# Optimization experiments

Measured on AMD Instinct MI355X. Metric: run time of the kernel, lower is better.

The kernel has to match this reference:

```python
import jax, jax.numpy as jnp
import numpy as np

B, N, F, H = 4, 40, 128, 128  # batch, num_nodes, in_features, hidden_features


def setup_inputs() -> dict:
    key = jax.random.key(0)
    ks = jax.random.split(key, 8)
    s = 0.02
    lengths = jax.random.randint(ks[0], (B,), N // 2, N + 1)
    mask = jnp.arange(N)[None, :] < lengths[:, None]  # (B, N) bool padding mask
    return dict(
        x=jax.random.normal(ks[1], (B, N, N, N, F), jnp.float32),
        mask=mask,
        Wi1=jax.random.normal(ks[2], (F, F), jnp.float32) * s, bi1=jnp.zeros((F,), jnp.float32),
        Wi2=jax.random.normal(ks[3], (F, H), jnp.float32) * s, bi2=jnp.zeros((H,), jnp.float32),
        We=jax.random.normal(ks[4], (H, H), jnp.float32) * s,
        Wo1=jax.random.normal(ks[5], (2 * H, 2 * H), jnp.float32) * s, bo1=jnp.zeros((2 * H,), jnp.float32),
        Wo2=jax.random.normal(ks[6], (2 * H, 1), jnp.float32) * s, bo2=jnp.zeros((1,), jnp.float32),
    )


def reference(x, mask, Wi1, bi1, Wi2, bi2, We, Wo1, bo1, Wo2, bo2):
    b, n = x.shape[0], x.shape[1]
    # inner MLP: F -> H, applied per hyperedge (B, n, n, n, H)
    x_embed = jnp.maximum(x @ Wi1 + bi1, 0.0) @ Wi2 + bi2
    # hyperedge validity: all three nodes unpadded AND strict ordering i < j < k
    idx = jnp.arange(n)
    ijk = (idx[:, None, None] < idx[None, :, None]) & (idx[None, :, None] < idx[None, None, :])  # (n,n,n)
    hm = (mask[:, :, None, None] & mask[:, None, :, None] & mask[:, None, None, :]) & ijk[None]  # (B,n,n,n)
    xf = x_embed.reshape(b, n * n * n, H)  # (B, n^3, H)
    logits = jnp.where(hm.reshape(b, n * n * n, 1), xf, -jnp.inf)
    a_flat = jax.nn.softmax(logits, axis=1)  # softmax over all n^3 hyperedges, per channel
    x_inner = jnp.maximum(xf @ We, 0.0)  # (B, n^3, H)
    h = jnp.concatenate([a_flat * x_inner, xf], axis=-1)  # (B, n^3, 2H)
    out = jnp.maximum(h @ Wo1 + bo1, 0.0) @ Wo2 + bo2  # (B, n^3, 1)
    return out.reshape(b, n, n, n)
```

## Files before the change

kernel.cpp:

```cpp
#include <hip/hip_runtime.h>

#define Bn 4
#define Nn 40
#define NCUBE 64000
#define ROWS 128
#define BPB  500
#define SROWS 64
#define SBPB 1000
#define MAXV 16384
#define CBLK 160

typedef _Float16 f16;
typedef __attribute__((ext_vector_type(8)))  _Float16 f16x8;
typedef __attribute__((ext_vector_type(4)))  _Float16 f16x4;
typedef __attribute__((ext_vector_type(4)))  float    f32x4;
typedef __attribute__((ext_vector_type(16))) float    f32x16;

#define OFF_WI1 0
#define OFF_WI2 16384
#define OFF_WE  32768
#define OFF_WO1 49152
#define WB_HALFS 114688
#define WB_BYTES (WB_HALFS*2)
#define WBOFF_COMPACT (4096 + Bn*MAXV*4)
#define WBOFF_SMALL   2560

__device__ __forceinline__ int swz8(int row, int colg) {
    return row*256 + (((colg & ~7) | ((colg ^ row) & 7)) << 3);
}
__device__ __forceinline__ int swzofs(int row, int col) {
    return swz8(row, col >> 3) + (col & 7);
}

template<bool PRE>
__device__ __forceinline__ f16x8 load_wfrag(const f16* __restrict__ WF,
                                            const float* __restrict__ W,
                                            int N, int NT, int kt, int nt, int l) {
    if constexpr (PRE) {
        return *(const f16x8*)(WF + ((kt*NT + nt)*64 + l)*8);
    } else {
        const int col = nt*32 + (l & 31);
        const int k0  = kt*16 + 8*(l >> 5);
        f16x8 r;
        #pragma unroll
        for (int j = 0; j < 8; ++j) r[j] = (f16)W[(k0 + j)*N + col];
        return r;
    }
}

__device__ __forceinline__ f16x8 lds_af(const f16* hb, int rowbase, int areag, int kt, int l) {
    return *(const f16x8*)&hb[swz8(rowbase + (l & 31), areag + 2*kt + (l >> 5))];
}

__global__ __launch_bounds__(256)
void prepcount_kernel(const float* __restrict__ Wi1, const float* __restrict__ Wi2,
                      const float* __restrict__ We,  const float* __restrict__ Wo1,
                      f16* __restrict__ WB, const unsigned char* __restrict__ mask,
                      int* __restrict__ cnt, int* __restrict__ vlist) {
    const int blk = blockIdx.x;
    if (blk < 56) {
        int id = blk*256 + threadIdx.x;
        const float* W; int NT, N; f16* WF; int fid;
        if (id < 2048)      { W = Wi1; NT = 4; N = 128; WF = WB+OFF_WI1; fid = id; }
        else if (id < 4096) { W = Wi2; NT = 4; N = 128; WF = WB+OFF_WI2; fid = id-2048; }
        else if (id < 6144) { W = We;  NT = 4; N = 128; WF = WB+OFF_WE;  fid = id-4096; }
        else                { W = Wo1; NT = 8; N = 256; WF = WB+OFF_WO1; fid = id-6144; }
        int frag = fid >> 6, l = fid & 63;
        int nt = frag % NT, kt = frag / NT;
        int col = nt*32 + (l & 31), k0 = kt*16 + 8*(l >> 5);
        #pragma unroll
        for (int j = 0; j < 8; ++j) WF[frag*512 + l*8 + j] = (f16)W[(k0 + j)*N + col];
    } else {
        const int idx = (blk - 56)*256 + threadIdx.x;
        const int b = idx / NCUBE, e = idx % NCUBE;
        const int k = e % Nn, ij = e / Nn, j = ij % Nn, i = ij / Nn;
        const bool v = (i < j) && (j < k) &&
                       mask[b*Nn+i] && mask[b*Nn+j] && mask[b*Nn+k];
        const unsigned long long m = __ballot(v);
        const int lane = threadIdx.x & 63;
        const int c = __popcll(m);
        int base = 0;
        if (lane == 0 && c) base = atomicAdd(&cnt[b], c);
        base = __shfl(base, 0);
        if (v) vlist[b*MAXV + base + __popcll(m & ((1ull<<lane)-1ull))] = e;
    }
}

template<bool PRE, bool COMPACT>
__global__ __launch_bounds__(512, 4)
void sums_kernel(const float* __restrict__ x, const unsigned char* __restrict__ mask,
                 const float* __restrict__ Wi1, const float* __restrict__ bi1,
                 const float* __restrict__ Wi2, const float* __restrict__ bi2,
                 float* __restrict__ sums, const int* __restrict__ cnt,
                 const int* __restrict__ vlist, const f16* __restrict__ WB)
{
    const int tid = threadIdx.x;
    const int l = tid & 63, w = tid >> 6, lr = l & 31, lh = l >> 5;
    const int wr = w >> 2, wc = w & 3;
    int b, r0;
    if (COMPACT) { b = blockIdx.x / CBLK; r0 = (blockIdx.x % CBLK)*SROWS; if (r0 >= cnt[b]) return; }
    else         { b = blockIdx.x / SBPB; r0 = (blockIdx.x % SBPB)*SROWS; }

    __shared__ __align__(16) f16 hb[SROWS*256];
    __shared__ int earr[SROWS];
    __shared__ unsigned char mlds[Nn];
    __shared__ int anyv;

    if (!COMPACT) { if (tid < Nn) mlds[tid] = mask[b*Nn + tid]; if (tid == 0) anyv = 0; }
    if (tid < SROWS) {
        if (COMPACT) { int r = r0 + tid; earr[tid] = (r < cnt[b]) ? vlist[b*MAXV + r] : -1; }
        else earr[tid] = r0 + tid;
    }
    __syncthreads();

    bool rv;
    {
        int e = earr[32*wr + lr];
        if (!COMPACT) {
            int k = e % Nn, ij = e / Nn, j = ij % Nn, i = ij / Nn;
            rv = (i < j) && (j < k) && mlds[i] && mlds[j] && mlds[k];
            if (__any(rv)) anyv = 1;
            __syncthreads();
            if (!anyv) return;
        } else rv = (e >= 0);
    }

    #pragma unroll
    for (int p = 0; p < 2; ++p) {
        const int row = p*32 + (tid >> 4);
        const int c0  = (tid & 15)*8;
        int e = earr[row]; if (e < 0) e = 0;
        const float4 x0 = *(const float4*)&x[((long)(b*NCUBE + e))*128 + c0];
        const float4 x1 = *(const float4*)&x[((long)(b*NCUBE + e))*128 + c0 + 4];
        f16x8 v; v[0]=(f16)x0.x; v[1]=(f16)x0.y; v[2]=(f16)x0.z; v[3]=(f16)x0.w;
                 v[4]=(f16)x1.x; v[5]=(f16)x1.y; v[6]=(f16)x1.z; v[7]=(f16)x1.w;
        *(f16x8*)&hb[swzofs(row, 128 + c0)] = v;
    }
    __syncthreads();

    f32x16 acc;
    #pragma unroll
    for (int rg = 0; rg < 4; ++rg) {
        const float4 bv = *(const float4*)(bi1 + 32*wc + 8*rg + 4*lh);
        acc[rg*4+0]=bv.x; acc[rg*4+1]=bv.y; acc[rg*4+2]=bv.z; acc[rg*4+3]=bv.w;
    }
    #pragma unroll
    for (int kt = 0; kt < 8; ++kt) {
        const f16x8 wf = load_wfrag<PRE>(WB+OFF_WI1, Wi1, 128, 4, kt, wc, l);
        const f16x8 af = lds_af(hb, 32*wr, 16, kt, l);
        acc = __builtin_amdgcn_mfma_f32_32x32x16_f16(wf, af, acc, 0, 0, 0);
    }
    #pragma unroll
    for (int rg = 0; rg < 4; ++rg) {
        f16x4 v;
        #pragma unroll
        for (int q = 0; q < 4; ++q) v[q] = (f16)fmaxf(acc[rg*4+q], 0.f);
        *(f16x4*)&hb[swzofs(32*wr + lr, 32*wc + 8*rg + 4*lh)] = v;
    }
    __syncthreads();

    #pragma unroll
    for (int rg = 0; rg < 4; ++rg) {
        const float4 bv = *(const float4*)(bi2 + 32*wc + 8*rg + 4*lh);
        acc[rg*4+0]=bv.x; acc[rg*4+1]=bv.y; acc[rg*4+2]=bv.z; acc[rg*4+3]=bv.w;
    }
    #pragma unroll
    for (int kt = 0; kt < 8; ++kt) {
        const f16x8 wf = load_wfrag<PRE>(WB+OFF_WI2, Wi2, 128, 4, kt, wc, l);
        const f16x8 af = lds_af(hb, 32*wr, 0, kt, l);
        acc = __builtin_amdgcn_mfma_f32_32x32x16_f16(wf, af, acc, 0, 0, 0);
    }

    float s[16];
    #pragma unroll
    for (int r = 0; r < 16; ++r) s[r] = rv ? __expf(acc[r]) : 0.0f;
    #pragma unroll
    for (int r = 0; r < 16; ++r) {
        float v = s[r];
        v += __shfl_xor(v, 1); v += __shfl_xor(v, 2);
        v += __shfl_xor(v, 4); v += __shfl_xor(v, 8); v += __shfl_xor(v, 16);
        if (lr == 0) atomicAdd(&sums[b*128 + 32*wc + 8*(r>>2) + 4*lh + (r&3)], v);
    }
}

template<bool PRE>
__global__ __launch_bounds__(512, 4)
void full_kernel(const float* __restrict__ x, const unsigned char* __restrict__ mask,
                 const float* __restrict__ Wi1, const float* __restrict__ bi1,
                 const float* __restrict__ Wi2, const float* __restrict__ bi2,
                 const float* __restrict__ We,
                 const float* __restrict__ Wo1, const float* __restrict__ bo1,
                 const float* __restrict__ Wo2, const float* __restrict__ bo2,
                 const float* __restrict__ sums, const f16* __restrict__ WB,
                 float* __restrict__ out)
{
    const int tid = threadIdx.x;
    const int l = tid & 63, w = tid >> 6, lr = l & 31, lh = l >> 5;
    const int wr = w >> 2, wc = w & 3;
    const int b = blockIdx.x / BPB;
    const int e0 = (blockIdx.x % BPB) * ROWS;

    __shared__ __align__(16) f16 hb[ROWS*256];
    __shared__ float red[8][64];
    __shared__ unsigned char mlds[Nn];

    if (tid < Nn) mlds[tid] = mask[b*Nn + tid];

    #pragma unroll
    for (int p = 0; p < 4; ++p) {
        const int row = p*32 + (tid >> 4);
        const int c0  = (tid & 15)*8;
        const long base = ((long)(b*NCUBE + e0 + row))*128 + c0;
        const float4 x0 = *(const float4*)&x[base];
        const float4 x1 = *(const float4*)&x[base + 4];
        f16x8 v; v[0]=(f16)x0.x; v[1]=(f16)x0.y; v[2]=(f16)x0.z; v[3]=(f16)x0.w;
                 v[4]=(f16)x1.x; v[5]=(f16)x1.y; v[6]=(f16)x1.z; v[7]=(f16)x1.w;
        *(f16x8*)&hb[swzofs(row, 128 + c0)] = v;
    }
    __syncthreads();

    bool valid[2];
    #pragma unroll
    for (int mt = 0; mt < 2; ++mt) {
        int e = e0 + 64*wr + 32*mt + lr;
        int k = e % Nn, ij = e / Nn, j = ij % Nn, i = ij / Nn;
        valid[mt] = (i < j) && (j < k) && mlds[i] && mlds[j] && mlds[k];
    }

    {
        f32x16 acc1[2];
        #pragma unroll
        for (int rg = 0; rg < 4; ++rg) {
            const float4 bv = *(const float4*)(bi1 + 32*wc + 8*rg + 4*lh);
            #pragma unroll
            for (int mt = 0; mt < 2; ++mt) {
                acc1[mt][rg*4+0]=bv.x; acc1[mt][rg*4+1]=bv.y;
                acc1[mt][rg*4+2]=bv.z; acc1[mt][rg*4+3]=bv.w;
            }
        }
        #pragma unroll
        for (int kt = 0; kt < 8; ++kt) {
            const f16x8 wf = load_wfrag<PRE>(WB+OFF_WI1, Wi1, 128, 4, kt, wc, l);
            #pragma unroll
            for (int mt = 0; mt < 2; ++mt) {
                const f16x8 af = lds_af(hb, 64*wr + 32*mt, 16, kt, l);
                acc1[mt] = __builtin_amdgcn_mfma_f32_32x32x16_f16(wf, af, acc1[mt], 0, 0, 0);
            }
        }
        #pragma unroll
        for (int mt = 0; mt < 2; ++mt)
            #pragma unroll
            for (int rg = 0; rg < 4; ++rg) {
                f16x4 v;
                #pragma unroll
                for (int q = 0; q < 4; ++q) v[q] = (f16)fmaxf(acc1[mt][rg*4+q], 0.f);
                *(f16x4*)&hb[swzofs(64*wr + 32*mt + lr, 32*wc + 8*rg + 4*lh)] = v;
            }
    }
    __syncthreads();

    f32x16 acc2[2];
    {
        #pragma unroll
        for (int rg = 0; rg < 4; ++rg) {
            const float4 bv = *(const float4*)(bi2 + 32*wc + 8*rg + 4*lh);
            #pragma unroll
            for (int mt = 0; mt < 2; ++mt) {
                acc2[mt][rg*4+0]=bv.x; acc2[mt][rg*4+1]=bv.y;
                acc2[mt][rg*4+2]=bv.z; acc2[mt][rg*4+3]=bv.w;
            }
        }
        #pragma unroll
        for (int kt = 0; kt < 8; ++kt) {
            const f16x8 wf = load_wfrag<PRE>(WB+OFF_WI2, Wi2, 128, 4, kt, wc, l);
            #pragma unroll
            for (int mt = 0; mt < 2; ++mt) {
                const f16x8 af = lds_af(hb, 64*wr + 32*mt, 0, kt, l);
                acc2[mt] = __builtin_amdgcn_mfma_f32_32x32x16_f16(wf, af, acc2[mt], 0, 0, 0);
            }
        }
        #pragma unroll
        for (int mt = 0; mt < 2; ++mt)
            #pragma unroll
            for (int rg = 0; rg < 4; ++rg) {
                f16x4 v;
                #pragma unroll
                for (int q = 0; q < 4; ++q) v[q] = (f16)acc2[mt][rg*4+q];
                *(f16x4*)&hb[swzofs(64*wr + 32*mt + lr, 128 + 32*wc + 8*rg + 4*lh)] = v;
            }
        #pragma unroll
        for (int rg = 0; rg < 4; ++rg) {
            const float4 sv = *(const float4*)(sums + b*128 + 32*wc + 8*rg + 4*lh);
            const float rinv[4] = {1.f/sv.x, 1.f/sv.y, 1.f/sv.z, 1.f/sv.w};
            #pragma unroll
            for (int mt = 0; mt < 2; ++mt)
                #pragma unroll
                for (int q = 0; q < 4; ++q)
                    acc2[mt][rg*4+q] = valid[mt] ? __expf(acc2[mt][rg*4+q]) * rinv[q] : 0.0f;
        }
    }
    __syncthreads();

    {
        f32x16 acc3[2];
        #pragma unroll
        for (int mt = 0; mt < 2; ++mt)
            #pragma unroll
            for (int r = 0; r < 16; ++r) acc3[mt][r] = 0.f;
        #pragma unroll
        for (int kt = 0; kt < 8; ++kt) {
            const f16x8 wf = load_wfrag<PRE>(WB+OFF_WE, We, 128, 4, kt, wc, l);
            #pragma unroll
            for (int mt = 0; mt < 2; ++mt) {
                const f16x8 af = lds_af(hb, 64*wr + 32*mt, 16, kt, l);
                acc3[mt] = __builtin_amdgcn_mfma_f32_32x32x16_f16(wf, af, acc3[mt], 0, 0, 0);
            }
        }
        #pragma unroll
        for (int mt = 0; mt < 2; ++mt)
            #pragma unroll
            for (int rg = 0; rg < 4; ++rg) {
                f16x4 v;
                #pragma unroll
                for (int q = 0; q < 4; ++q)
                    v[q] = (f16)(acc2[mt][rg*4+q] * fmaxf(acc3[mt][rg*4+q], 0.f));
                *(f16x4*)&hb[swzofs(64*wr + 32*mt + lr, 32*wc + 8*rg + 4*lh)] = v;
            }
    }
    __syncthreads();

    f32x16 acc4[2][2];
    #pragma unroll
    for (int ntl = 0; ntl < 2; ++ntl)
        #pragma unroll
        for (int rg = 0; rg < 4; ++rg) {
            const float4 bv = *(const float4*)(bo1 + 64*wc + 32*ntl + 8*rg + 4*lh);
            #pragma unroll
            for (int mt = 0; mt < 2; ++mt) {
                acc4[mt][ntl][rg*4+0]=bv.x; acc4[mt][ntl][rg*4+1]=bv.y;
                acc4[mt][ntl][rg*4+2]=bv.z; acc4[mt][ntl][rg*4+3]=bv.w;
            }
        }
    #pragma unroll
    for (int kt = 0; kt < 16; ++kt) {
        f16x8 of0 = load_wfrag<PRE>(WB+OFF_WO1, Wo1, 256, 8, kt, 2*wc+0, l);
        f16x8 of1 = load_wfrag<PRE>(WB+OFF_WO1, Wo1, 256, 8, kt, 2*wc+1, l);
        #pragma unroll
        for (int mt = 0; mt < 2; ++mt) {
            const f16x8 af = lds_af(hb, 64*wr + 32*mt, 0, kt, l);
            acc4[mt][0] = __builtin_amdgcn_mfma_f32_32x32x16_f16(of0, af, acc4[mt][0], 0, 0, 0);
            acc4[mt][1] = __builtin_amdgcn_mfma_f32_32x32x16_f16(of1, af, acc4[mt][1], 0, 0, 0);
        }
    }

    {
        float outp[2] = {0.f, 0.f};
        #pragma unroll
        for (int ntl = 0; ntl < 2; ++ntl)
            #pragma unroll
            for (int rg = 0; rg < 4; ++rg) {
                const float4 wv = *(const float4*)(Wo2 + 64*wc + 32*ntl + 8*rg + 4*lh);
                #pragma unroll
                for (int mt = 0; mt < 2; ++mt) {
                    outp[mt] += fmaxf(acc4[mt][ntl][rg*4+0], 0.f)*wv.x
                              + fmaxf(acc4[mt][ntl][rg*4+1], 0.f)*wv.y
                              + fmaxf(acc4[mt][ntl][rg*4+2], 0.f)*wv.z
                              + fmaxf(acc4[mt][ntl][rg*4+3], 0.f)*wv.w;
                }
            }
        #pragma unroll
        for (int mt = 0; mt < 2; ++mt) outp[mt] += __shfl_xor(outp[mt], 32);
        if (l < 32) {
            red[w][lr]      = outp[0];
            red[w][32 + lr] = outp[1];
        }
        __syncthreads();
        if (tid < ROWS) {
            const int wr2 = tid >> 6, idx = tid & 63;
            out[(long)b*NCUBE + e0 + tid] =
                red[wr2*4+0][idx] + red[wr2*4+1][idx] +
                red[wr2*4+2][idx] + red[wr2*4+3][idx] + bo2[0];
        }
    }
}

extern "C" void kernel_launch(void* const* d_in, const int* in_sizes, int n_in,
                              void* d_out, int out_size, void* d_ws, size_t ws_size,
                              hipStream_t stream) {
    const float*         x    = (const float*)d_in[0];
    const unsigned char* mask = (const unsigned char*)d_in[1];
    const float* Wi1 = (const float*)d_in[2];
    const float* bi1 = (const float*)d_in[3];
    const float* Wi2 = (const float*)d_in[4];
    const float* bi2 = (const float*)d_in[5];
    const float* We  = (const float*)d_in[6];
    const float* Wo1 = (const float*)d_in[7];
    const float* bo1 = (const float*)d_in[8];
    const float* Wo2 = (const float*)d_in[9];
    const float* bo2 = (const float*)d_in[10];
    float* out  = (float*)d_out;
    float* sums = (float*)d_ws;
    int*   cnt   = (int*)((char*)d_ws + 2048);
    int*   vlist = (int*)((char*)d_ws + 4096);

    const bool compact = ws_size >= (size_t)(WBOFF_COMPACT + WB_BYTES);
    const size_t wboff = compact ? WBOFF_COMPACT : WBOFF_SMALL;
    const bool pre     = ws_size >= wboff + WB_BYTES;
    f16* WB = (f16*)((char*)d_ws + wboff);

    hipMemsetAsync(d_ws, 0, 2048 + Bn*sizeof(int), stream);

    if (compact) {
        prepcount_kernel<<<1056, 256, 0, stream>>>(Wi1, Wi2, We, Wo1, WB, mask, cnt, vlist);
        sums_kernel<true, true><<<Bn*CBLK, 512, 0, stream>>>(x, mask, Wi1, bi1, Wi2, bi2,
                                                             sums, cnt, vlist, WB);
        full_kernel<true><<<Bn*BPB, 512, 0, stream>>>(x, mask, Wi1, bi1, Wi2, bi2, We,
                                                      Wo1, bo1, Wo2, bo2, sums, WB, out);
    } else if (pre) {
        prepcount_kernel<<<56, 256, 0, stream>>>(Wi1, Wi2, We, Wo1, WB, mask, cnt, vlist);
        sums_kernel<true, false><<<Bn*SBPB, 512, 0, stream>>>(x, mask, Wi1, bi1, Wi2, bi2,
                                                              sums, cnt, vlist, WB);
        full_kernel<true><<<Bn*BPB, 512, 0, stream>>>(x, mask, Wi1, bi1, Wi2, bi2, We,
                                                      Wo1, bo1, Wo2, bo2, sums, WB, out);
    } else {
        sums_kernel<false, false><<<Bn*SBPB, 512, 0, stream>>>(x, mask, Wi1, bi1, Wi2, bi2,
                                                               sums, cnt, vlist, WB);
        full_kernel<false><<<Bn*BPB, 512, 0, stream>>>(x, mask, Wi1, bi1, Wi2, bi2, We,
                                                       Wo1, bo1, Wo2, bo2, sums, WB, out);
    }
}
```

Measured before the change: 271.1 us.

## Compute embeddings once and store fp16 xf to workspace for output pass

Replaces the compacted valid-row sums pass with an embed kernel that reads x once for every row, computes the inner MLP, accumulates the softmax denominators and writes the fp16 embeddings to a large workspace buffer. A new output kernel reads those fp16 embeddings instead of re-reading the fp32 x and recomputing the inner MLP. This removes the second fp32 read of x and the duplicated Wi1/Wi2 GEMMs. In exchange it needs a workspace of about 65 MB plus an extra fp16 write and read, and the embed pass now covers all rows rather than only the valid ones.

```diff
diff --git a/kernel.cpp b/kernel.cpp
--- a/kernel.cpp
+++ b/kernel.cpp
@@ -7,13 +7,10 @@
 #define BPB  500
 #define SROWS 64
 #define SBPB 1000
-#define MAXV 16384
-#define CBLK 160
 
 typedef _Float16 f16;
 typedef __attribute__((ext_vector_type(8)))  _Float16 f16x8;
 typedef __attribute__((ext_vector_type(4)))  _Float16 f16x4;
-typedef __attribute__((ext_vector_type(4)))  float    f32x4;
 typedef __attribute__((ext_vector_type(16))) float    f32x16;
 
 #define OFF_WI1 0
@@ -22,8 +19,10 @@
 #define OFF_WO1 49152
 #define WB_HALFS 114688
 #define WB_BYTES (WB_HALFS*2)
-#define WBOFF_COMPACT (4096 + Bn*MAXV*4)
-#define WBOFF_SMALL   2560
+#define XF_BYTES (Bn*NCUBE*128*2)
+#define WBOFF_BIG (2048 + XF_BYTES)
+#define WS_BIG    (WBOFF_BIG + WB_BYTES)
+#define WBOFF_SMALL 2560
 
 __device__ __forceinline__ int swz8(int row, int colg) {
     return row*256 + (((colg & ~7) | ((colg ^ row) & 7)) << 3);
@@ -52,86 +51,282 @@
     return *(const f16x8*)&hb[swz8(rowbase + (l & 31), areag + 2*kt + (l >> 5))];
 }
 
+__device__ __forceinline__ bool row_valid(int e, const unsigned char* mlds) {
+    int k = e % Nn, ij = e / Nn, j = ij % Nn, i = ij / Nn;
+    return (i < j) && (j < k) && mlds[i] && mlds[j] && mlds[k];
+}
+
 __global__ __launch_bounds__(256)
-void prepcount_kernel(const float* __restrict__ Wi1, const float* __restrict__ Wi2,
-                      const float* __restrict__ We,  const float* __restrict__ Wo1,
-                      f16* __restrict__ WB, const unsigned char* __restrict__ mask,
-                      int* __restrict__ cnt, int* __restrict__ vlist) {
-    const int blk = blockIdx.x;
-    if (blk < 56) {
-        int id = blk*256 + threadIdx.x;
-        const float* W; int NT, N; f16* WF; int fid;
-        if (id < 2048)      { W = Wi1; NT = 4; N = 128; WF = WB+OFF_WI1; fid = id; }
-        else if (id < 4096) { W = Wi2; NT = 4; N = 128; WF = WB+OFF_WI2; fid = id-2048; }
-        else if (id < 6144) { W = We;  NT = 4; N = 128; WF = WB+OFF_WE;  fid = id-4096; }
-        else                { W = Wo1; NT = 8; N = 256; WF = WB+OFF_WO1; fid = id-6144; }
-        int frag = fid >> 6, l = fid & 63;
-        int nt = frag % NT, kt = frag / NT;
-        int col = nt*32 + (l & 31), k0 = kt*16 + 8*(l >> 5);
-        #pragma unroll
-        for (int j = 0; j < 8; ++j) WF[frag*512 + l*8 + j] = (f16)W[(k0 + j)*N + col];
-    } else {
-        const int idx = (blk - 56)*256 + threadIdx.x;
-        const int b = idx / NCUBE, e = idx % NCUBE;
-        const int k = e % Nn, ij = e / Nn, j = ij % Nn, i = ij / Nn;
-        const bool v = (i < j) && (j < k) &&
-                       mask[b*Nn+i] && mask[b*Nn+j] && mask[b*Nn+k];
-        const unsigned long long m = __ballot(v);
-        const int lane = threadIdx.x & 63;
-        const int c = __popcll(m);
-        int base = 0;
-        if (lane == 0 && c) base = atomicAdd(&cnt[b], c);
-        base = __shfl(base, 0);
-        if (v) vlist[b*MAXV + base + __popcll(m & ((1ull<<lane)-1ull))] = e;
-    }
-}
-
-template<bool PRE, bool COMPACT>
+void prep_kernel(const float* __restrict__ Wi1, const float* __restrict__ Wi2,
+                 const float* __restrict__ We,  const float* __restrict__ Wo1,
+                 f16* __restrict__ WB) {
+    int id = blockIdx.x*256 + threadIdx.x;
+    const float* W; int NT, N; f16* WF; int fid;
+    if (id < 2048)      { W = Wi1; NT = 4; N = 128; WF = WB+OFF_WI1; fid = id; }
+    else if (id < 4096) { W = Wi2; NT = 4; N = 128; WF = WB+OFF_WI2; fid = id-2048; }
+    else if (id < 6144) { W = We;  NT = 4; N = 128; WF = WB+OFF_WE;  fid = id-4096; }
+    else                { W = Wo1; NT = 8; N = 256; WF = WB+OFF_WO1; fid = id-6144; }
+    int frag = fid >> 6, l = fid & 63;
+    int nt = frag % NT, kt = frag / NT;
+    int col = nt*32 + (l & 31), k0 = kt*16 + 8*(l >> 5);
+    #pragma unroll
+    for (int j = 0; j < 8; ++j) WF[frag*512 + l*8 + j] = (f16)W[(k0 + j)*N + col];
+}
+
+template<bool PRE>
+__global__ __launch_bounds__(512, 4)
+void embed_kernel(const float* __restrict__ x, const unsigned char* __restrict__ mask,
+                  const float* __restrict__ Wi1, const float* __restrict__ bi1,
+                  const float* __restrict__ Wi2, const float* __restrict__ bi2,
+                  float* __restrict__ sums, f16* __restrict__ xfg,
+                  const f16* __restrict__ WB)
+{
+    const int tid = threadIdx.x;
+    const int l = tid & 63, w = tid >> 6, lr = l & 31, lh = l >> 5;
+    const int wr = w >> 2, wc = w & 3;
+    const int b = blockIdx.x / SBPB;
+    const int e0 = (blockIdx.x % SBPB) * SROWS;
+
+    __shared__ __align__(16) f16 hb[SROWS*256];
+    __shared__ unsigned char mlds[Nn];
+
+    if (tid < Nn) mlds[tid] = mask[b*Nn + tid];
+
+    #pragma unroll
+    for (int p = 0; p < 2; ++p) {
+        const int row = p*32 + (tid >> 4);
+        const int c0  = (tid & 15)*8;
+        const long base = ((long)(b*NCUBE + e0 + row))*128 + c0;
+        const float4 x0 = *(const float4*)&x[base];
+        const float4 x1 = *(const float4*)&x[base + 4];
+        f16x8 v; v[0]=(f16)x0.x; v[1]=(f16)x0.y; v[2]=(f16)x0.z; v[3]=(f16)x0.w;
+                 v[4]=(f16)x1.x; v[5]=(f16)x1.y; v[6]=(f16)x1.z; v[7]=(f16)x1.w;
+        *(f16x8*)&hb[swzofs(row, 128 + c0)] = v;
+    }
+    __syncthreads();
+
+    const bool rv = row_valid(e0 + 32*wr + lr, mlds);
+
+    f32x16 acc;
+    #pragma unroll
+    for (int rg = 0; rg < 4; ++rg) {
+        const float4 bv = *(const float4*)(bi1 + 32*wc + 8*rg + 4*lh);
+        acc[rg*4+0]=bv.x; acc[rg*4+1]=bv.y; acc[rg*4+2]=bv.z; acc[rg*4+3]=bv.w;
+    }
+    #pragma unroll
+    for (int kt = 0; kt < 8; ++kt) {
+        const f16x8 wf = load_wfrag<PRE>(WB+OFF_WI1, Wi1, 128, 4, kt, wc, l);
+        const f16x8 af = lds_af(hb, 32*wr, 16, kt, l);
+        acc = __builtin_amdgcn_mfma_f32_32x32x16_f16(wf, af, acc, 0, 0, 0);
+    }
+    #pragma unroll
+    for (int rg = 0; rg < 4; ++rg) {
+        f16x4 v;
+        #pragma unroll
+        for (int q = 0; q < 4; ++q) v[q] = (f16)fmaxf(acc[rg*4+q], 0.f);
+        *(f16x4*)&hb[swzofs(32*wr + lr, 32*wc + 8*rg + 4*lh)] = v;
+    }
+    __syncthreads();
+
+    #pragma unroll
+    for (int rg = 0; rg < 4; ++rg) {
+        const float4 bv = *(const float4*)(bi2 + 32*wc + 8*rg + 4*lh);
+        acc[rg*4+0]=bv.x; acc[rg*4+1]=bv.y; acc[rg*4+2]=bv.z; acc[rg*4+3]=bv.w;
+    }
+    #pragma unroll
+    for (int kt = 0; kt < 8; ++kt) {
+        const f16x8 wf = load_wfrag<PRE>(WB+OFF_WI2, Wi2, 128, 4, kt, wc, l);
+        const f16x8 af = lds_af(hb, 32*wr, 0, kt, l);
+        acc = __builtin_amdgcn_mfma_f32_32x32x16_f16(wf, af, acc, 0, 0, 0);
+    }
+
+    float s[16];
+    #pragma unroll
+    for (int rg = 0; rg < 4; ++rg) {
+        f16x4 v;
+        #pragma unroll
+        for (int q = 0; q < 4; ++q) {
+            v[q] = (f16)acc[rg*4+q];
+            s[rg*4+q] = rv ? __expf((float)v[q]) : 0.0f;
+        }
+        *(f16x4*)&hb[swzofs(32*wr + lr, 128 + 32*wc + 8*rg + 4*lh)] = v;
+    }
+    #pragma unroll
+    for (int r = 0; r < 16; ++r) {
+        float v = s[r];
+        v += __shfl_xor(v, 1); v += __shfl_xor(v, 2);
+        v += __shfl_xor(v, 4); v += __shfl_xor(v, 8); v += __shfl_xor(v, 16);
+        if (lr == 0) atomicAdd(&sums[b*128 + 32*wc + 8*(r>>2) + 4*lh + (r&3)], v);
+    }
+    __syncthreads();
+
+    #pragma unroll
+    for (int p = 0; p < 2; ++p) {
+        const int row = p*32 + (tid >> 4);
+        const int c0  = (tid & 15)*8;
+        const f16x8 v = *(const f16x8*)&hb[swzofs(row, 128 + c0)];
+        *(f16x8*)&xfg[((long)(b*NCUBE + e0 + row))*128 + c0] = v;
+    }
+}
+
+template<bool PRE>
+__global__ __launch_bounds__(512, 4)
+void out_kernel(const f16* __restrict__ xfg, const unsigned char* __restrict__ mask,
+                const float* __restrict__ We,
+                const float* __restrict__ Wo1, const float* __restrict__ bo1,
+                const float* __restrict__ Wo2, const float* __restrict__ bo2,
+                const float* __restrict__ sums, const f16* __restrict__ WB,
+                float* __restrict__ out)
+{
+    const int tid = threadIdx.x;
+    const int l = tid & 63, w = tid >> 6, lr = l & 31, lh = l >> 5;
+    const int wr = w >> 2, wc = w & 3;
+    const int b = blockIdx.x / BPB;
+    const int e0 = (blockIdx.x % BPB) * ROWS;
+
+    __shared__ __align__(16) f16 hb[ROWS*256];
+    __shared__ float red[8][64];
+    __shared__ unsigned char mlds[Nn];
+
+    if (tid < Nn) mlds[tid] = mask[b*Nn + tid];
+
+    #pragma unroll
+    for (int p = 0; p < 4; ++p) {
+        const int row = p*32 + (tid >> 4);
+        const int c0  = (tid & 15)*8;
+        const f16x8 v = *(const f16x8*)&xfg[((long)(b*NCUBE + e0 + row))*128 + c0];
+        *(f16x8*)&hb[swzofs(row, 128 + c0)] = v;
+    }
+    __syncthreads();
+
+    bool valid[2];
+    #pragma unroll
+    for (int mt = 0; mt < 2; ++mt)
+        valid[mt] = row_valid(e0 + 64*wr + 32*mt + lr, mlds);
+
+    {
+        f32x16 acc3[2];
+        #pragma unroll
+        for (int mt = 0; mt < 2; ++mt)
+            #pragma unroll
+            for (int r = 0; r < 16; ++r) acc3[mt][r] = 0.f;
+        #pragma unroll
+        for (int kt = 0; kt < 8; ++kt) {
+            const f16x8 wf = load_wfrag<PRE>(WB+OFF_WE, We, 128, 4, kt, wc, l);
+            #pragma unroll
+            for (int mt = 0; mt < 2; ++mt) {
+                const f16x8 af = lds_af(hb, 64*wr + 32*mt, 16, kt, l);
+                acc3[mt] = __builtin_amdgcn_mfma_f32_32x32x16_f16(wf, af, acc3[mt], 0, 0, 0);
+            }
+        }
+        #pragma unroll
+        for (int rg = 0; rg < 4; ++rg) {
+            const float4 sv = *(const float4*)(sums + b*128 + 32*wc + 8*rg + 4*lh);
+            const float rinv[4] = {1.f/sv.x, 1.f/sv.y, 1.f/sv.z, 1.f/sv.w};
+            #pragma unroll
+            for (int mt = 0; mt < 2; ++mt) {
+                const f16x4 xq = *(const f16x4*)&hb[swzofs(64*wr + 32*mt + lr,
+                                                           128 + 32*wc + 8*rg + 4*lh)];
+                f16x4 v;
+                #pragma unroll
+                for (int q = 0; q < 4; ++q) {
+                    const float aa = valid[mt] ? __expf((float)xq[q]) * rinv[q] : 0.0f;
+                    v[q] = (f16)(aa * fmaxf(acc3[mt][rg*4+q], 0.f));
+                }
+                *(f16x4*)&hb[swzofs(64*wr + 32*mt + lr, 32*wc + 8*rg + 4*lh)] = v;
+            }
+        }
+    }
+    __syncthreads();
+
+    f32x16 acc4[2][2];
+    #pragma unroll
+    for (int ntl = 0; ntl < 2; ++ntl)
+        #pragma unroll
+        for (int rg = 0; rg < 4; ++rg) {
+            const float4 bv = *(const float4*)(bo1 + 64*wc + 32*ntl + 8*rg + 4*lh);
+            #pragma unroll
+            for (int mt = 0; mt < 2; ++mt) {
+                acc4[mt][ntl][rg*4+0]=bv.x; acc4[mt][ntl][rg*4+1]=bv.y;
+                acc4[mt][ntl][rg*4+2]=bv.z; acc4[mt][ntl][rg*4+3]=bv.w;
+            }
+        }
+    #pragma unroll
+    for (int kt = 0; kt < 16; ++kt) {
+        f16x8 of0 = load_wfrag<PRE>(WB+OFF_WO1, Wo1, 256, 8, kt, 2*wc+0, l);
+        f16x8 of1 = load_wfrag<PRE>(WB+OFF_WO1, Wo1, 256, 8, kt, 2*wc+1, l);
+        #pragma unroll
+        for (int mt = 0; mt < 2; ++mt) {
+            const f16x8 af = lds_af(hb, 64*wr + 32*mt, 0, kt, l);
+            acc4[mt][0] = __builtin_amdgcn_mfma_f32_32x32x16_f16(of0, af, acc4[mt][0], 0, 0, 0);
+            acc4[mt][1] = __builtin_amdgcn_mfma_f32_32x32x16_f16(of1, af, acc4[mt][1], 0, 0, 0);
+        }
+    }
+
+    {
+        float outp[2] = {0.f, 0.f};
+        #pragma unroll
+        for (int ntl = 0; ntl < 2; ++ntl)
+            #pragma unroll
+            for (int rg = 0; rg < 4; ++rg) {
+                const float4 wv = *(const float4*)(Wo2 + 64*wc + 32*ntl + 8*rg + 4*lh);
+                #pragma unroll
+                for (int mt = 0; mt < 2; ++mt) {
+                    outp[mt] += fmaxf(acc4[mt][ntl][rg*4+0], 0.f)*wv.x
+                              + fmaxf(acc4[mt][ntl][rg*4+1], 0.f)*wv.y
+                              + fmaxf(acc4[mt][ntl][rg*4+2], 0.f)*wv.z
+                              + fmaxf(acc4[mt][ntl][rg*4+3], 0.f)*wv.w;
+                }
+            }
+        #pragma unroll
+        for (int mt = 0; mt < 2; ++mt) outp[mt] += __shfl_xor(outp[mt], 32);
+        if (l < 32) {
+            red[w][lr]      = outp[0];
+            red[w][32 + lr] = outp[1];
+        }
+        __syncthreads();
+        if (tid < ROWS) {
+            const int wr2 = tid >> 6, idx = tid & 63;
+            out[(long)b*NCUBE + e0 + tid] =
+                red[wr2*4+0][idx] + red[wr2*4+1][idx] +
+                red[wr2*4+2][idx] + red[wr2*4+3][idx] + bo2[0];
+        }
+    }
+}
+
+template<bool PRE>
 __global__ __launch_bounds__(512, 4)
 void sums_kernel(const float* __restrict__ x, const unsigned char* __restrict__ mask,
                  const float* __restrict__ Wi1, const float* __restrict__ bi1,
                  const float* __restrict__ Wi2, const float* __restrict__ bi2,
-                 float* __restrict__ sums, const int* __restrict__ cnt,
-                 const int* __restrict__ vlist, const f16* __restrict__ WB)
+                 float* __restrict__ sums, const f16* __restrict__ WB)
 {
     const int tid = threadIdx.x;
     const int l = tid & 63, w = tid >> 6, lr = l & 31, lh = l >> 5;
     const int wr = w >> 2, wc = w & 3;
-    int b, r0;
-    if (COMPACT) { b = blockIdx.x / CBLK; r0 = (blockIdx.x % CBLK)*SROWS; if (r0 >= cnt[b]) return; }
-    else         { b = blockIdx.x / SBPB; r0 = (blockIdx.x % SBPB)*SROWS; }
+    const int b = blockIdx.x / SBPB;
+    const int e0 = (blockIdx.x % SBPB) * SROWS;
 
     __shared__ __align__(16) f16 hb[SROWS*256];
-    __shared__ int earr[SROWS];
     __shared__ unsigned char mlds[Nn];
     __shared__ int anyv;
 
-    if (!COMPACT) { if (tid < Nn) mlds[tid] = mask[b*Nn + tid]; if (tid == 0) anyv = 0; }
-    if (tid < SROWS) {
-        if (COMPACT) { int r = r0 + tid; earr[tid] = (r < cnt[b]) ? vlist[b*MAXV + r] : -1; }
-        else earr[tid] = r0 + tid;
-    }
-    __syncthreads();
-
-    bool rv;
-    {
-        int e = earr[32*wr + lr];
-        if (!COMPACT) {
-            int k = e % Nn, ij = e / Nn, j = ij % Nn, i = ij / Nn;
-            rv = (i < j) && (j < k) && mlds[i] && mlds[j] && mlds[k];
-            if (__any(rv)) anyv = 1;
-            __syncthreads();
-            if (!anyv) return;
-        } else rv = (e >= 0);
-    }
+    if (tid < Nn) mlds[tid] = mask[b*Nn + tid];
+    if (tid == 0) anyv = 0;
+    __syncthreads();
+
+    const bool rv = row_valid(e0 + 32*wr + lr, mlds);
+    if (__any(rv)) anyv = 1;
+    __syncthreads();
+    if (!anyv) return;
 
     #pragma unroll
     for (int p = 0; p < 2; ++p) {
         const int row = p*32 + (tid >> 4);
         const int c0  = (tid & 15)*8;
-        int e = earr[row]; if (e < 0) e = 0;
-        const float4 x0 = *(const float4*)&x[((long)(b*NCUBE + e))*128 + c0];
-        const float4 x1 = *(const float4*)&x[((long)(b*NCUBE + e))*128 + c0 + 4];
+        const long base = ((long)(b*NCUBE + e0 + row))*128 + c0;
+        const float4 x0 = *(const float4*)&x[base];
+        const float4 x1 = *(const float4*)&x[base + 4];
         f16x8 v; v[0]=(f16)x0.x; v[1]=(f16)x0.y; v[2]=(f16)x0.z; v[3]=(f16)x0.w;
                  v[4]=(f16)x1.x; v[5]=(f16)x1.y; v[6]=(f16)x1.z; v[7]=(f16)x1.w;
         *(f16x8*)&hb[swzofs(row, 128 + c0)] = v;
@@ -221,11 +416,8 @@
 
     bool valid[2];
     #pragma unroll
-    for (int mt = 0; mt < 2; ++mt) {
-        int e = e0 + 64*wr + 32*mt + lr;
-        int k = e % Nn, ij = e / Nn, j = ij % Nn, i = ij / Nn;
-        valid[mt] = (i < j) && (j < k) && mlds[i] && mlds[j] && mlds[k];
-    }
+    for (int mt = 0; mt < 2; ++mt)
+        valid[mt] = row_valid(e0 + 64*wr + 32*mt + lr, mlds);
 
     {
         f32x16 acc1[2];
@@ -400,32 +592,27 @@
     const float* bo2 = (const float*)d_in[10];
     float* out  = (float*)d_out;
     float* sums = (float*)d_ws;
-    int*   cnt   = (int*)((char*)d_ws + 2048);
-    int*   vlist = (int*)((char*)d_ws + 4096);
-
-    const bool compact = ws_size >= (size_t)(WBOFF_COMPACT + WB_BYTES);
-    const size_t wboff = compact ? WBOFF_COMPACT : WBOFF_SMALL;
-    const bool pre     = ws_size >= wboff + WB_BYTES;
-    f16* WB = (f16*)((char*)d_ws + wboff);
-
-    hipMemsetAsync(d_ws, 0, 2048 + Bn*sizeof(int), stream);
-
-    if (compact) {
-        prepcount_kernel<<<1056, 256, 0, stream>>>(Wi1, Wi2, We, Wo1, WB, mask, cnt, vlist);
-        sums_kernel<true, true><<<Bn*CBLK, 512, 0, stream>>>(x, mask, Wi1, bi1, Wi2, bi2,
-                                                             sums, cnt, vlist, WB);
-        full_kernel<true><<<Bn*BPB, 512, 0, stream>>>(x, mask, Wi1, bi1, Wi2, bi2, We,
-                                                      Wo1, bo1, Wo2, bo2, sums, WB, out);
-    } else if (pre) {
-        prepcount_kernel<<<56, 256, 0, stream>>>(Wi1, Wi2, We, Wo1, WB, mask, cnt, vlist);
-        sums_kernel<true, false><<<Bn*SBPB, 512, 0, stream>>>(x, mask, Wi1, bi1, Wi2, bi2,
-                                                              sums, cnt, vlist, WB);
+
+    hipMemsetAsync(d_ws, 0, 2048, stream);
+
+    if (ws_size >= (size_t)WS_BIG) {
+        f16* xfg = (f16*)((char*)d_ws + 2048);
+        f16* WB  = (f16*)((char*)d_ws + WBOFF_BIG);
+        prep_kernel<<<56, 256, 0, stream>>>(Wi1, Wi2, We, Wo1, WB);
+        embed_kernel<true><<<Bn*SBPB, 512, 0, stream>>>(x, mask, Wi1, bi1, Wi2, bi2,
+                                                        sums, xfg, WB);
+        out_kernel<true><<<Bn*BPB, 512, 0, stream>>>(xfg, mask, We, Wo1, bo1, Wo2, bo2,
+                                                     sums, WB, out);
+    } else if (ws_size >= (size_t)(WBOFF_SMALL + WB_BYTES)) {
+        f16* WB = (f16*)((char*)d_ws + WBOFF_SMALL);
+        prep_kernel<<<56, 256, 0, stream>>>(Wi1, Wi2, We, Wo1, WB);
+        sums_kernel<true><<<Bn*SBPB, 512, 0, stream>>>(x, mask, Wi1, bi1, Wi2, bi2, sums, WB);
         full_kernel<true><<<Bn*BPB, 512, 0, stream>>>(x, mask, Wi1, bi1, Wi2, bi2, We,
                                                       Wo1, bo1, Wo2, bo2, sums, WB, out);
     } else {
-        sums_kernel<false, false><<<Bn*SBPB, 512, 0, stream>>>(x, mask, Wi1, bi1, Wi2, bi2,
-                                                               sums, cnt, vlist, WB);
+        sums_kernel<false><<<Bn*SBPB, 512, 0, stream>>>(x, mask, Wi1, bi1, Wi2, bi2,
+                                                        sums, nullptr);
         full_kernel<false><<<Bn*BPB, 512, 0, stream>>>(x, mask, Wi1, bi1, Wi2, bi2, We,
-                                                       Wo1, bo1, Wo2, bo2, sums, WB, out);
-    }
-}
+                                                       Wo1, bo1, Wo2, bo2, sums, nullptr, out);
+    }
+}
```

Measured after the change: 1.021 ms. 277% more time.
